# Optimization experiments

Hardware: AMD Instinct MI355X
Metric: run time of the kernel (lower is better)

The kernel has to match this reference:

```python
import jax, jax.numpy as jnp
import numpy as np

B, T, F = 8, 2048, 512          # batch, seq, input_dim
G, E = 2, 320                   # num_codebooks, num_codebook_entries
D = 768 // G                    # entry_dim = output_dim // num_codebooks = 384
TAU = 2.0                       # max_temp * decay**0 (num_updates == 0)
EPS = 1e-7


def setup_inputs() -> dict:
    key = jax.random.key(0)
    k1, k2, k3, k4 = jax.random.split(key, 4)
    x = jax.random.normal(k1, (B, T, F), dtype=jnp.float32)
    proj_w = jax.random.normal(k2, (G * E, F), dtype=jnp.float32)  # init: normal(0,1)
    proj_b = jnp.zeros((G * E,), dtype=jnp.float32)                 # init: zeros
    entries = jax.random.uniform(k3, (1, G * E, D), dtype=jnp.float32)  # init: uniform
    u = jax.random.uniform(k4, (B * T * G, E), dtype=jnp.float32,
                           minval=1e-10, maxval=1.0)
    gumbel = -jnp.log(-jnp.log(u))  # standard Gumbel noise, fixed for determinism
    return {"x": x, "proj_w": proj_w, "proj_b": proj_b,
            "entries": entries, "gumbel": gumbel}


def reference(x, proj_w, proj_b, entries, gumbel):
    N = B * T
    # entry projection: (B,T,F) @ (F, G*E) -> logits over all codebook entries
    logits = jnp.einsum("btf,ef->bte", x, proj_w) + proj_b  # (B,T,G*E)
    logits = logits.reshape(N * G, E)

    # hard one-hot by argmax (code perplexity)
    k = jnp.argmax(logits, axis=-1)
    hard_x = jax.nn.one_hot(k, E, dtype=logits.dtype).reshape(N, G, E)
    hard_probs = jnp.mean(hard_x, axis=0)  # (G,E)
    code_perplexity = jnp.sum(
        jnp.exp(-jnp.sum(hard_probs * jnp.log(hard_probs + EPS), axis=-1)))

    # soft probabilities (prob perplexity)
    avg_probs = jnp.mean(
        jax.nn.softmax(logits.reshape(N, G, E), axis=-1), axis=0)  # (G,E)
    prob_perplexity = jnp.sum(
        jnp.exp(-jnp.sum(avg_probs * jnp.log(avg_probs + EPS), axis=-1)))

    # gumbel_softmax(tau=TAU, hard=True), training path, straight-through
    y_soft = jax.nn.softmax((logits + gumbel) / TAU, axis=-1)  # (N*G, E)
    idx = jnp.argmax(y_soft, axis=-1)
    y_hard = jax.nn.one_hot(idx, E, dtype=y_soft.dtype)
    y = y_hard - jax.lax.stop_gradient(y_soft) + y_soft

    cb = y.reshape(N, G * E)
    # combine: equivalent to (cb[:, :, None] * entries).view(N,G,E,D).sum(-2)
    quantized = jnp.einsum(
        "nge,ged->ngd", y.reshape(N, G, E), entries.reshape(G, E, D))
    quantized = quantized.reshape(B, T, G * D)  # (B,T,768)

    return quantized, cb, code_perplexity, prob_perplexity
```

## Files before the change

kernel.cpp:

```cpp
#include <hip/hip_runtime.h>
#include <hip/hip_bf16.h>

typedef unsigned short ushort_t;
typedef __attribute__((ext_vector_type(8))) short bf16x8;
typedef __attribute__((ext_vector_type(4))) float f32x4;

#define NROWS 16384
#define FDIM  512
#define GE    640
#define EDIM  320
#define DDIM  384
#define CB_OFF 12582912
#define SCAL_OFF 23068672
#define XB_OFF 0
#define WB_OFF 4194304


#define SLOT_OFF 1280
#define SLOT_BIG_ROWS 2048
#define SLOT_SMALL_COPIES 64

__global__ void vq_init_k(float* acc, int n) {
    int i = blockIdx.x * 256 + threadIdx.x;
    if (i < n) acc[i] = 0.0f;
}

static __device__ __forceinline__ unsigned f2bf(float f) {
    unsigned u = __float_as_uint(f);
    return (u + 0x7FFFu + ((u >> 16) & 1u)) >> 16;
}

__global__ __launch_bounds__(256) void convert_bf16_k(
    const float* __restrict__ X, const float* __restrict__ W,
    ushort_t* __restrict__ Xb, ushort_t* __restrict__ Wb)
{
    const size_t i = (size_t)blockIdx.x * 256 + threadIdx.x;
    const float4* src;
    ushort_t* dst;
    if (i < 1048576) {
        src = (const float4*)X + i * 2;
        dst = Xb + i * 8;
    } else {
        const size_t j = i - 1048576;
        src = (const float4*)W + j * 2;
        dst = Wb + j * 8;
    }
    const float4 v0 = src[0], v1 = src[1];
    uint4 o;
    o.x = f2bf(v0.x) | (f2bf(v0.y) << 16);
    o.y = f2bf(v0.z) | (f2bf(v0.w) << 16);
    o.z = f2bf(v1.x) | (f2bf(v1.y) << 16);
    o.w = f2bf(v1.z) | (f2bf(v1.w) << 16);
    *(uint4*)dst = o;
}

static __device__ __forceinline__ void gload16(const void* g, void* l) {
    __builtin_amdgcn_global_load_lds(
        (const __attribute__((address_space(1))) unsigned int*)g,
        (__attribute__((address_space(3))) unsigned int*)l, 16, 0, 0);
}

__global__ __launch_bounds__(256) void gemm_mfma_k(
    const ushort_t* __restrict__ Xb, const ushort_t* __restrict__ Wb,
    const float* __restrict__ bias, float* __restrict__ L)
{
    __shared__ __align__(16) ushort_t As[128 * 32];
    __shared__ __align__(16) ushort_t Bs[128 * 32];

    const int tid  = threadIdx.x;
    const int lane = tid & 63;
    const int wv   = tid >> 6;
    const int wr   = (wv >> 1) * 64;
    const int wc   = (wv & 1) * 64;
    const int row0 = blockIdx.x * 128;
    const int col0 = blockIdx.y * 128;

    const int c0r = tid >> 2;
    const int c0k = (tid & 3) * 8;

    f32x4 acc[4][4] = {};

    const int rA = lane & 15;
    const int kb = (lane >> 4) * 8;

    for (int t = 0; t < 16; ++t) {
        const int k0 = t * 32;
        gload16(Xb + (size_t)(row0 + c0r) * FDIM + k0 + c0k,        &As[tid * 8]);
        gload16(Xb + (size_t)(row0 + 64 + c0r) * FDIM + k0 + c0k,   &As[2048 + tid * 8]);
        gload16(Wb + (size_t)(col0 + c0r) * FDIM + k0 + c0k,        &Bs[tid * 8]);
        gload16(Wb + (size_t)(col0 + 64 + c0r) * FDIM + k0 + c0k,   &Bs[2048 + tid * 8]);
        __syncthreads();

        bf16x8 af[4], bfr[4];
        #pragma unroll
        for (int mi = 0; mi < 4; ++mi)
            af[mi] = *(const bf16x8*)&As[(wr + mi * 16 + rA) * 32 + kb];
        #pragma unroll
        for (int ni = 0; ni < 4; ++ni)
            bfr[ni] = *(const bf16x8*)&Bs[(wc + ni * 16 + rA) * 32 + kb];

        #pragma unroll
        for (int mi = 0; mi < 4; ++mi)
            #pragma unroll
            for (int ni = 0; ni < 4; ++ni)
                acc[mi][ni] = __builtin_amdgcn_mfma_f32_16x16x32_bf16(
                    af[mi], bfr[ni], acc[mi][ni], 0, 0, 0);
        __syncthreads();
    }

    const int colb = col0 + wc + (lane & 15);
    const int rowb = row0 + wr + (lane >> 4) * 4;
    #pragma unroll
    for (int ni = 0; ni < 4; ++ni) {
        const int col = colb + ni * 16;
        const float bv = bias[col];
        #pragma unroll
        for (int mi = 0; mi < 4; ++mi) {
            const int row = rowb + mi * 16;
            #pragma unroll
            for (int j = 0; j < 4; ++j) {
                ushort_t* lrow = (ushort_t*)(L + (size_t)(row + j) * GE + 320);
                lrow[col] = (ushort_t)f2bf(acc[mi][ni][j] + bv);
            }
        }
    }
}

__global__ __launch_bounds__(256, 6) void vq_fused_k(
    float* __restrict__ Lcb,
    const float* __restrict__ gumbel,
    const float* __restrict__ entries,
    float* __restrict__ qout,
    float* __restrict__ red_hard,
    float* __restrict__ slotS,
    int mode)
{
    __shared__ float part[4][320];
    __shared__ float yv_a[16];
    __shared__ int   gi_a[16];

    const int tid  = threadIdx.x;
    const int lane = tid & 63;
    const int w    = tid >> 6;
    const int r    = lane & 3;
    const int o    = lane >> 2;
    const int u    = w * 4 + r;
    const int g    = u >> 3;
    const int nr   = u & 7;
    const int n0   = blockIdx.x * 8;
    const int n    = n0 + nr;

    const ushort_t* lrow16 = (const ushort_t*)(Lcb + (size_t)n * GE + 320) + g * EDIM;
    const float* grow = gumbel + ((size_t)n * 2 + g) * EDIM;

    f32x4 l4[5], g4[5];
    #pragma unroll
    for (int s = 0; s < 5; ++s) {
        const ushort4 lu = *(const ushort4*)(lrow16 + s * 64 + o * 4);
        l4[s][0] = __uint_as_float((unsigned)lu.x << 16);
        l4[s][1] = __uint_as_float((unsigned)lu.y << 16);
        l4[s][2] = __uint_as_float((unsigned)lu.z << 16);
        l4[s][3] = __uint_as_float((unsigned)lu.w << 16);
        g4[s] = *(const f32x4*)(grow + s * 64 + o * 4);
    }

    float mh = -3.4e38f, mg = -3.4e38f;
    int hi = 0, gi = 0;
    #pragma unroll
    for (int s = 0; s < 5; ++s) {
        #pragma unroll
        for (int k = 0; k < 4; ++k) {
            const float lv = l4[s][k];
            const float tv = (lv + g4[s][k]) * 0.5f;
            const int e = s * 64 + o * 4 + k;
            if (lv > mh) { mh = lv; hi = e; }
            if (tv > mg) { mg = tv; gi = e; }
        }
    }
    #pragma unroll
    for (int off = 4; off < 64; off <<= 1) {
        const float om = __shfl_xor(mh, off); const int oi = __shfl_xor(hi, off);
        if (om > mh || (om == mh && oi < hi)) { mh = om; hi = oi; }
        const float om2 = __shfl_xor(mg, off); const int oi2 = __shfl_xor(gi, off);
        if (om2 > mg || (om2 == mg && oi2 < gi)) { mg = om2; gi = oi2; }
    }

    f32x4 eh[5];
    float sh = 0.f, sg = 0.f;
    #pragma unroll
    for (int s = 0; s < 5; ++s) {
        f32x4 e4;
        #pragma unroll
        for (int k = 0; k < 4; ++k) {
            const float lv = l4[s][k];
            const float tv = (lv + g4[s][k]) * 0.5f;
            const float ev = __expf(lv - mh);
            e4[k] = ev;
            sh += ev;
            sg += __expf(tv - mg);
        }
        eh[s] = e4;
    }
    #pragma unroll
    for (int off = 4; off < 64; off <<= 1) {
        sh += __shfl_xor(sh, off);
        sg += __shfl_xor(sg, off);
    }
    const float ish = 1.0f / sh;
    const float isg = 1.0f / sg;
    const float yv  = (1.0f - isg) + isg;

    if (o == 0) {
        yv_a[u] = yv;
        gi_a[u] = gi;
        atomicAdd(&red_hard[g * EDIM + hi], 1.0f);
    }

    #pragma unroll
    for (int s = 0; s < 5; ++s) {
        f32x4 p4;
        #pragma unroll
        for (int k = 0; k < 4; ++k) p4[k] = eh[s][k] * ish;
        #pragma unroll
        for (int off = 1; off < 4; off <<= 1) {
            #pragma unroll
            for (int k = 0; k < 4; ++k) p4[k] += __shfl_xor(p4[k], off);
        }
        if (r == 0) *(f32x4*)&part[w][s * 64 + o * 4] = p4;
    }
    __syncthreads();

    #pragma unroll
    for (int it = 0; it < 5; ++it) {
        const int idx = it * 256 + tid;
        const int rr  = idx / 160;
        const int c4  = idx % 160;
        const int gg  = (c4 >= 80) ? 1 : 0;
        const int e4  = (c4 - gg * 80) * 4;
        const int uu  = gg * 8 + rr;
        const int gii = gi_a[uu];
        const float yvv = yv_a[uu];
        f32x4 cv;
        #pragma unroll
        for (int k = 0; k < 4; ++k) cv[k] = (e4 + k == gii) ? yvv : 0.0f;
        *(f32x4*)(Lcb + (size_t)(n0 + rr) * GE + c4 * 4) = cv;
    }

    #pragma unroll
    for (int it = 0; it < 6; ++it) {
        const int idx = it * 256 + tid;
        const int rr  = idx / 192;
        const int c4  = idx % 192;
        const int gg  = (c4 >= 96) ? 1 : 0;
        const int d4  = (c4 - gg * 96) * 4;
        const int uu  = gg * 8 + rr;
        const int gii = gi_a[uu];
        const float yvv = yv_a[uu];
        const f32x4 ev = *(const f32x4*)(entries + ((size_t)(gg * EDIM + gii)) * DDIM + d4);
        f32x4 qv;
        #pragma unroll
        for (int k = 0; k < 4; ++k) qv[k] = yvv * ev[k];
        *(f32x4*)(qout + (size_t)(n0 + rr) * 768 + c4 * 4) = qv;
    }

    for (int e = tid; e < 640; e += 256) {
        const int gg = e / 320, ee = e % 320;
        const float s = part[gg * 2][ee] + part[gg * 2 + 1][ee];
        if (mode == 1) {
            slotS[(size_t)blockIdx.x * 640 + e] = s;
        } else {
            atomicAdd(&slotS[(size_t)(blockIdx.x & (SLOT_SMALL_COPIES - 1)) * 640 + e], s);
        }
    }
}

__global__ __launch_bounds__(256) void reduce_soft3_k(
    const float* __restrict__ slotS, int nrows, float* __restrict__ red_soft)
{
    const int gid = blockIdx.x * 256 + threadIdx.x;
    const int nchunk = nrows / 32;
    if (gid >= 640 * nchunk) return;
    const int col   = gid % 640;
    const int chunk = gid / 640;
    const int base  = chunk * 32;
    float a0 = 0.f, a1 = 0.f, a2 = 0.f, a3 = 0.f;
    #pragma unroll
    for (int k = 0; k < 32; k += 4) {
        a0 += slotS[(size_t)(base + k + 0) * 640 + col];
        a1 += slotS[(size_t)(base + k + 1) * 640 + col];
        a2 += slotS[(size_t)(base + k + 2) * 640 + col];
        a3 += slotS[(size_t)(base + k + 3) * 640 + col];
    }
    atomicAdd(&red_soft[col], (a0 + a1) + (a2 + a3));
}

__global__ void vq_final_k(const float* __restrict__ red_hard,
                           const float* __restrict__ red_soft,
                           float* __restrict__ out)
{
    const int lane = threadIdx.x & 63;
    float code = 0.f, prob = 0.f;
    for (int g = 0; g < 2; ++g) {
        float shh = 0.f, sss = 0.f;
        #pragma unroll
        for (int j = 0; j < 5; ++j) {
            const int e = g * EDIM + lane + j * 64;
            const float ph = red_hard[e] * (1.0f / 16384.0f);
            const float ps = red_soft[e] * (1.0f / 16384.0f);
            shh += ph * __logf(ph + 1e-7f);
            sss += ps * __logf(ps + 1e-7f);
        }
        #pragma unroll
        for (int off = 32; off > 0; off >>= 1) {
            shh += __shfl_xor(shh, off);
            sss += __shfl_xor(sss, off);
        }
        code += __expf(-shh);
        prob += __expf(-sss);
    }
    if (threadIdx.x == 0) {
        out[SCAL_OFF + 0] = code;
        out[SCAL_OFF + 1] = prob;
    }
}

extern "C" void kernel_launch(void* const* d_in, const int* in_sizes, int n_in,
                              void* d_out, int out_size, void* d_ws, size_t ws_size,
                              hipStream_t stream) {
    const float* x       = (const float*)d_in[0];
    const float* proj_w  = (const float*)d_in[1];
    const float* proj_b  = (const float*)d_in[2];
    const float* entries = (const float*)d_in[3];
    const float* gumbel  = (const float*)d_in[4];
    float* out = (float*)d_out;
    float* ws  = (float*)d_ws;
    float* cb = out + CB_OFF;
    ushort_t* Xb = (ushort_t*)(out + XB_OFF);
    ushort_t* Wb = (ushort_t*)(out + WB_OFF);

    float* red_hard = ws;
    float* red_soft = ws + 640;
    float* slotS    = ws + SLOT_OFF;

    const size_t need1 = (size_t)(SLOT_OFF + SLOT_BIG_ROWS * 640) * 4;
    const int mode  = (ws_size >= need1) ? 1 : 0;
    const int nrows = (mode == 1) ? SLOT_BIG_ROWS : SLOT_SMALL_COPIES;
    const int nz = (mode == 1) ? 1280 : (SLOT_OFF + SLOT_SMALL_COPIES * 640);
    const int redblocks = (640 * (nrows / 32) + 255) / 256;

    hipLaunchKernelGGL(vq_init_k, dim3((nz + 255) / 256), dim3(256), 0, stream,
                       ws, nz);
    hipLaunchKernelGGL(convert_bf16_k, dim3(4256), dim3(256), 0, stream,
                       x, proj_w, Xb, Wb);
    hipLaunchKernelGGL(gemm_mfma_k, dim3(NROWS / 128, GE / 128), dim3(256), 0, stream,
                       Xb, Wb, proj_b, cb);
    hipLaunchKernelGGL(vq_fused_k, dim3(2048), dim3(256), 0, stream,
                       cb, gumbel, entries, out, red_hard, slotS, mode);
    hipLaunchKernelGGL(reduce_soft3_k, dim3(redblocks), dim3(256), 0, stream,
                       slotS, nrows, red_soft);
    hipLaunchKernelGGL(vq_final_k, dim3(1), dim3(64), 0, stream,
                       red_hard, red_soft, out);
}
```

Before: 75.87 us.

## Fuse X bf16 conversion into GEMM and halve VQ block size

Drops the separate pass that converted all of X to bf16. The GEMM now loads fp32 X tiles directly and packs them to bf16 in registers before storing to LDS, which removes a full write and re-read of X in bf16. Only W is still converted by a small kernel. The VQ kernel moves to 128-thread blocks handling 4 rows each, with a tiered slot scheme for the soft-probability partial sums; this doubles the slot rows when workspace allows. The trade-off is that X loads in the GEMM now go through registers synchronously instead of async global-to-LDS, which may expose load latency.

After: 83.75 us. 10.4% more time.

```diff
diff --git a/kernel.cpp b/kernel.cpp
--- a/kernel.cpp
+++ b/kernel.cpp
@@ -12,13 +12,10 @@
 #define DDIM  384
 #define CB_OFF 12582912
 #define SCAL_OFF 23068672
-#define XB_OFF 0
-#define WB_OFF 4194304
+#define WB_OFF 0
 
 
 #define SLOT_OFF 1280
-#define SLOT_BIG_ROWS 2048
-#define SLOT_SMALL_COPIES 64
 
 __global__ void vq_init_k(float* acc, int n) {
     int i = blockIdx.x * 256 + threadIdx.x;
@@ -30,28 +27,23 @@
     return (u + 0x7FFFu + ((u >> 16) & 1u)) >> 16;
 }
 
-__global__ __launch_bounds__(256) void convert_bf16_k(
-    const float* __restrict__ X, const float* __restrict__ W,
-    ushort_t* __restrict__ Xb, ushort_t* __restrict__ Wb)
-{
-    const size_t i = (size_t)blockIdx.x * 256 + threadIdx.x;
-    const float4* src;
-    ushort_t* dst;
-    if (i < 1048576) {
-        src = (const float4*)X + i * 2;
-        dst = Xb + i * 8;
-    } else {
-        const size_t j = i - 1048576;
-        src = (const float4*)W + j * 2;
-        dst = Wb + j * 8;
-    }
-    const float4 v0 = src[0], v1 = src[1];
+static __device__ __forceinline__ uint4 pack8(const float4 v0, const float4 v1) {
     uint4 o;
     o.x = f2bf(v0.x) | (f2bf(v0.y) << 16);
     o.y = f2bf(v0.z) | (f2bf(v0.w) << 16);
     o.z = f2bf(v1.x) | (f2bf(v1.y) << 16);
     o.w = f2bf(v1.z) | (f2bf(v1.w) << 16);
-    *(uint4*)dst = o;
+    return o;
+}
+
+__global__ __launch_bounds__(256) void convert_w_k(
+    const float* __restrict__ W, ushort_t* __restrict__ Wb)
+{
+    const int i = blockIdx.x * 256 + threadIdx.x;
+    if (i >= 40960) return;
+    const float4 v0 = ((const float4*)W)[i * 2];
+    const float4 v1 = ((const float4*)W)[i * 2 + 1];
+    *(uint4*)(Wb + (size_t)i * 8) = pack8(v0, v1);
 }
 
 static __device__ __forceinline__ void gload16(const void* g, void* l) {
@@ -61,7 +53,7 @@
 }
 
 __global__ __launch_bounds__(256) void gemm_mfma_k(
-    const ushort_t* __restrict__ Xb, const ushort_t* __restrict__ Wb,
+    const float* __restrict__ X, const ushort_t* __restrict__ Wb,
     const float* __restrict__ bias, float* __restrict__ L)
 {
     __shared__ __align__(16) ushort_t As[128 * 32];
@@ -85,10 +77,14 @@
 
     for (int t = 0; t < 16; ++t) {
         const int k0 = t * 32;
-        gload16(Xb + (size_t)(row0 + c0r) * FDIM + k0 + c0k,        &As[tid * 8]);
-        gload16(Xb + (size_t)(row0 + 64 + c0r) * FDIM + k0 + c0k,   &As[2048 + tid * 8]);
-        gload16(Wb + (size_t)(col0 + c0r) * FDIM + k0 + c0k,        &Bs[tid * 8]);
-        gload16(Wb + (size_t)(col0 + 64 + c0r) * FDIM + k0 + c0k,   &Bs[2048 + tid * 8]);
+        const float4 a0 = *(const float4*)(X + (size_t)(row0 + c0r) * FDIM + k0 + c0k);
+        const float4 a1 = *(const float4*)(X + (size_t)(row0 + c0r) * FDIM + k0 + c0k + 4);
+        const float4 a2 = *(const float4*)(X + (size_t)(row0 + 64 + c0r) * FDIM + k0 + c0k);
+        const float4 a3 = *(const float4*)(X + (size_t)(row0 + 64 + c0r) * FDIM + k0 + c0k + 4);
+        gload16(Wb + (size_t)(col0 + c0r) * FDIM + k0 + c0k,      &Bs[tid * 8]);
+        gload16(Wb + (size_t)(col0 + 64 + c0r) * FDIM + k0 + c0k, &Bs[2048 + tid * 8]);
+        *(uint4*)&As[c0r * 32 + c0k]        = pack8(a0, a1);
+        *(uint4*)&As[(64 + c0r) * 32 + c0k] = pack8(a2, a3);
         __syncthreads();
 
         bf16x8 af[4], bfr[4];
@@ -126,18 +122,18 @@
     }
 }
 
-__global__ __launch_bounds__(256, 6) void vq_fused_k(
+__global__ __launch_bounds__(128, 8) void vq_fused_k(
     float* __restrict__ Lcb,
     const float* __restrict__ gumbel,
     const float* __restrict__ entries,
     float* __restrict__ qout,
     float* __restrict__ red_hard,
     float* __restrict__ slotS,
-    int mode)
-{
-    __shared__ float part[4][320];
-    __shared__ float yv_a[16];
-    __shared__ int   gi_a[16];
+    int tier)
+{
+    __shared__ float part[2][320];
+    __shared__ float yv_a[8];
+    __shared__ int   gi_a[8];
 
     const int tid  = threadIdx.x;
     const int lane = tid & 63;
@@ -145,9 +141,9 @@
     const int r    = lane & 3;
     const int o    = lane >> 2;
     const int u    = w * 4 + r;
-    const int g    = u >> 3;
-    const int nr   = u & 7;
-    const int n0   = blockIdx.x * 8;
+    const int g    = u >> 2;
+    const int nr   = u & 3;
+    const int n0   = blockIdx.x * 4;
     const int n    = n0 + nr;
 
     const ushort_t* lrow16 = (const ushort_t*)(Lcb + (size_t)n * GE + 320) + g * EDIM;
@@ -232,12 +228,12 @@
 
     #pragma unroll
     for (int it = 0; it < 5; ++it) {
-        const int idx = it * 256 + tid;
+        const int idx = it * 128 + tid;
         const int rr  = idx / 160;
         const int c4  = idx % 160;
         const int gg  = (c4 >= 80) ? 1 : 0;
         const int e4  = (c4 - gg * 80) * 4;
-        const int uu  = gg * 8 + rr;
+        const int uu  = gg * 4 + rr;
         const int gii = gi_a[uu];
         const float yvv = yv_a[uu];
         f32x4 cv;
@@ -248,12 +244,12 @@
 
     #pragma unroll
     for (int it = 0; it < 6; ++it) {
-        const int idx = it * 256 + tid;
+        const int idx = it * 128 + tid;
         const int rr  = idx / 192;
         const int c4  = idx % 192;
         const int gg  = (c4 >= 96) ? 1 : 0;
         const int d4  = (c4 - gg * 96) * 4;
-        const int uu  = gg * 8 + rr;
+        const int uu  = gg * 4 + rr;
         const int gii = gi_a[uu];
         const float yvv = yv_a[uu];
         const f32x4 ev = *(const f32x4*)(entries + ((size_t)(gg * EDIM + gii)) * DDIM + d4);
@@ -263,14 +259,12 @@
         *(f32x4*)(qout + (size_t)(n0 + rr) * 768 + c4 * 4) = qv;
     }
 
-    for (int e = tid; e < 640; e += 256) {
+    for (int e = tid; e < 640; e += 128) {
         const int gg = e / 320, ee = e % 320;
-        const float s = part[gg * 2][ee] + part[gg * 2 + 1][ee];
-        if (mode == 1) {
-            slotS[(size_t)blockIdx.x * 640 + e] = s;
-        } else {
-            atomicAdd(&slotS[(size_t)(blockIdx.x & (SLOT_SMALL_COPIES - 1)) * 640 + e], s);
-        }
+        const float s = part[gg][ee];
+        if (tier == 2)      slotS[(size_t)blockIdx.x * 640 + e] = s;
+        else if (tier == 1) atomicAdd(&slotS[(size_t)(blockIdx.x & 2047) * 640 + e], s);
+        else                atomicAdd(&slotS[(size_t)(blockIdx.x & 63) * 640 + e], s);
     }
 }
 
@@ -335,27 +329,27 @@
     float* out = (float*)d_out;
     float* ws  = (float*)d_ws;
     float* cb = out + CB_OFF;
-    ushort_t* Xb = (ushort_t*)(out + XB_OFF);
     ushort_t* Wb = (ushort_t*)(out + WB_OFF);
 
     float* red_hard = ws;
     float* red_soft = ws + 640;
     float* slotS    = ws + SLOT_OFF;
 
-    const size_t need1 = (size_t)(SLOT_OFF + SLOT_BIG_ROWS * 640) * 4;
-    const int mode  = (ws_size >= need1) ? 1 : 0;
-    const int nrows = (mode == 1) ? SLOT_BIG_ROWS : SLOT_SMALL_COPIES;
-    const int nz = (mode == 1) ? 1280 : (SLOT_OFF + SLOT_SMALL_COPIES * 640);
+    const size_t needA = (size_t)(SLOT_OFF + 4096 * 640) * 4;
+    const size_t needB = (size_t)(SLOT_OFF + 2048 * 640) * 4;
+    const int tier  = (ws_size >= needA) ? 2 : (ws_size >= needB) ? 1 : 0;
+    const int nrows = (tier == 2) ? 4096 : (tier == 1) ? 2048 : 64;
+    const int nz = (tier == 2) ? 1280 : (SLOT_OFF + nrows * 640);
     const int redblocks = (640 * (nrows / 32) + 255) / 256;
 
     hipLaunchKernelGGL(vq_init_k, dim3((nz + 255) / 256), dim3(256), 0, stream,
                        ws, nz);
-    hipLaunchKernelGGL(convert_bf16_k, dim3(4256), dim3(256), 0, stream,
-                       x, proj_w, Xb, Wb);
+    hipLaunchKernelGGL(convert_w_k, dim3(160), dim3(256), 0, stream,
+                       proj_w, Wb);
     hipLaunchKernelGGL(gemm_mfma_k, dim3(NROWS / 128, GE / 128), dim3(256), 0, stream,
-                       Xb, Wb, proj_b, cb);
-    hipLaunchKernelGGL(vq_fused_k, dim3(2048), dim3(256), 0, stream,
-                       cb, gumbel, entries, out, red_hard, slotS, mode);
+                       x, Wb, proj_b, cb);
+    hipLaunchKernelGGL(vq_fused_k, dim3(4096), dim3(128), 0, stream,
+                       cb, gumbel, entries, out, red_hard, slotS, tier);
     hipLaunchKernelGGL(reduce_soft3_k, dim3(redblocks), dim3(256), 0, stream,
                        slotS, nrows, red_soft);
     hipLaunchKernelGGL(vq_final_k, dim3(1), dim3(64), 0, stream,
```
